# Kernel tuning notes

Measured on AMD Instinct MI355X. Metric: run time of the kernel, lower is better.

The kernel has to match this reference:

```python
import jax, jax.numpy as jnp
import numpy as np

B = 4          # per_gpu_batch_size
P = 16         # n_contexts
N = B * P      # fused passage dim = 64
L = 512        # seq_len
H = 768        # hidden_size
S = 16         # sentence spans per passage


def setup_inputs() -> dict:
    key = jax.random.key(0)
    k1, k2, k3 = jax.random.split(key, 3)
    hidden_states = jax.random.normal(k1, (N, L, H), jnp.float32)
    # nn.Linear weight [out, in]; original init std=1.0 saturates tanh, use 0.02 scale for sane numerics
    dense_w = jax.random.normal(k2, (H, H), jnp.float32) * 0.02
    dense_b = jnp.zeros((H,), jnp.float32)
    attention_mask = jnp.ones((N, L), jnp.int32)
    # strictly increasing boundaries -> S non-empty, ragged, contiguous spans per passage
    r = jnp.sort(jax.random.randint(k3, (N, S + 1), 0, L - S), axis=-1) + jnp.arange(S + 1, dtype=jnp.int32)
    spans = jnp.stack([r[:, :-1], r[:, 1:]], axis=-1).astype(jnp.int32)  # [N, S, 2]
    return dict(hidden_states=hidden_states, dense_w=dense_w, dense_b=dense_b,
                attention_mask=attention_mask, spans=spans)


def reference(hidden_states, dense_w, dense_b, attention_mask, spans):
    # sentence_spans branch: token_tensor = hidden_states (all tokens)
    # pooled_output = activation(dense(token_tensor)); cls_norm_type == 'none' -> no norm
    pooled = jnp.tanh(jnp.einsum('nlh,oh->nlo', hidden_states, dense_w) + dense_b)  # [N, L, H]
    pooled_output_passages = pooled[:, 0]  # [N, H]
    # ragged per-span mean pooling, vectorized as a masked segment reduce
    pos = jnp.arange(L, dtype=jnp.int32)                         # [L]
    start = spans[..., 0][..., None]                             # [N, S, 1]
    end = spans[..., 1][..., None]                               # [N, S, 1]
    m = ((pos >= start) & (pos < end)).astype(pooled.dtype)      # [N, S, L]
    sums = jnp.einsum('nsl,nlh->nsh', m, pooled)                 # [N, S, H]
    counts = (spans[..., 1] - spans[..., 0]).astype(pooled.dtype)[..., None]  # [N, S, 1]
    sentence_embeddings = (sums / counts).reshape(N * S, H)      # [N*S, H]
    # all S spans valid per passage -> mask of zeros (0 = valid in original code)
    sentence_mask = jnp.zeros((N, S), jnp.float32)
    return pooled_output_passages, sentence_embeddings, sentence_mask
```

## Files before the change

kernel.cpp:

```cpp
#include <hip/hip_runtime.h>
#include <hip/hip_bf16.h>

#define NPASS 64
#define LSEQ  512
#define HDIM  768
#define NSPAN 16
#define MTOT  (NPASS*LSEQ)
#define OFF_SENT (NPASS*HDIM)
#define OFF_MASK (OFF_SENT + NPASS*NSPAN*HDIM)
#define W_ELEMS (HDIM*HDIM)

#define BM   64
#define BK   32
#define NK   (HDIM/BK)
#define NBLK (MTOT/BM)
#define THREADS 512
#define NMT  2
#define NTN  12

typedef __bf16 bf16x8 __attribute__((ext_vector_type(8)));
typedef __bf16 bf16x4 __attribute__((ext_vector_type(4)));
typedef float  f32x4  __attribute__((ext_vector_type(4)));

__device__ inline unsigned short f2bf(float f) {
  __hip_bfloat16 h = __float2bfloat16(f);
  unsigned short u; __builtin_memcpy(&u, &h, 2); return u;
}

__device__ inline float fast_tanh(float x) {
  const float ax = fabsf(x);
  const float t  = __expf(-2.0f * ax);
  const float r  = (1.0f - t) * __builtin_amdgcn_rcpf(1.0f + t);
  return copysignf(r, x);
}

__device__ inline bf16x8 cvt8(f32x4 lo, f32x4 hi) {
  union { bf16x4 h[2]; bf16x8 v; } u;
  u.h[0] = __builtin_convertvector(lo, bf16x4);
  u.h[1] = __builtin_convertvector(hi, bf16x4);
  return u.v;
}

__global__ __launch_bounds__(256) void convert_w_kernel(
    const float* __restrict__ W, unsigned short* __restrict__ Wb)
{
  const int i = (blockIdx.x * 256 + threadIdx.x) * 8;
  const float4 a = *(const float4*)(W + i);
  const float4 b = *(const float4*)(W + i + 4);
  union { unsigned short us[8]; uint4 v; } o;
  o.us[0]=f2bf(a.x); o.us[1]=f2bf(a.y); o.us[2]=f2bf(a.z); o.us[3]=f2bf(a.w);
  o.us[4]=f2bf(b.x); o.us[5]=f2bf(b.y); o.us[6]=f2bf(b.z); o.us[7]=f2bf(b.w);
  *(uint4*)(Wb + i) = o.v;
}

__global__ __launch_bounds__(THREADS, 2) void gemm_fused_kernel(
    const float* __restrict__ A,
    const unsigned short* __restrict__ Wb,
    const float* __restrict__ bias,
    const int* __restrict__ spans,
    float* __restrict__ out)
{
  __shared__ __align__(16) float          As[2][BM*BK];
  __shared__ __align__(16) unsigned short Ws[2][HDIM*BK];
  __shared__ float inv_s[NSPAN];
  __shared__ float bias_s[HDIM];
  __shared__ short sid_l[BM];

  const int tid  = threadIdx.x;
  const int b    = blockIdx.x;
  const int p    = b >> 3;
  const int l0   = (b & 7) << 6;
  const int row0 = b * BM;

  const int wave = tid >> 6;
  const int lane = tid & 63;
  const int quad = lane >> 4;
  const int lr   = lane & 15;
  const int mr   = wave >> 2;
  const int nw   = wave & 3;

  auto stage = [&](int k, int buf) {
    const int k0 = k * BK;
    {
      const int row = wave * 8 + (lane >> 3);
      const int g   = (lane & 7) ^ ((lane >> 3) & 7);
      const float* src = A + (size_t)(row0 + row) * HDIM + (k0 + g * 4);
      __builtin_amdgcn_global_load_lds(
          (const __attribute__((address_space(1))) void*)src,
          (__attribute__((address_space(3))) void*)(As[buf] + wave * 256),
          16, 0, 0);
    }
    #pragma unroll
    for (int j = 0; j < 6; ++j) {
      const int s2  = wave * 6 + j;
      const int row = s2 * 16 + (lane >> 2);
      const int g   = (lane & 3) ^ ((lane >> 2) & 3);
      const unsigned short* src = Wb + (size_t)row * HDIM + (k0 + g * 8);
      __builtin_amdgcn_global_load_lds(
          (const __attribute__((address_space(1))) void*)src,
          (__attribute__((address_space(3))) void*)(Ws[buf] + s2 * 512),
          16, 0, 0);
    }
  };

  stage(0, 0);
  if (tid < NSPAN)
    inv_s[tid] = 1.0f / (float)(spans[(p * NSPAN + tid) * 2 + 1] -
                                spans[(p * NSPAN + tid) * 2 + 0]);
  if (tid < BM) {
    const int l = l0 + tid;
    short s = -1;
    #pragma unroll
    for (int i = 0; i < NSPAN; ++i) {
      const int st = spans[(p * NSPAN + i) * 2 + 0];
      const int en = spans[(p * NSPAN + i) * 2 + 1];
      if (l >= st && l < en) s = (short)i;
    }
    sid_l[tid] = s;
  }
  for (int i = tid; i < HDIM; i += THREADS) bias_s[i] = bias[i];
  __syncthreads();

  f32x4 acc[NMT][NTN];
  #pragma unroll
  for (int mt = 0; mt < NMT; ++mt)
    #pragma unroll
    for (int nt = 0; nt < NTN; ++nt)
      acc[mt][nt] = (f32x4){0.f, 0.f, 0.f, 0.f};

  for (int k = 0; k < NK; ++k) {
    const int cur = k & 1;
    if (k + 1 < NK) stage(k + 1, cur ^ 1);

    bf16x8 abf[NMT];
    #pragma unroll
    for (int mt = 0; mt < NMT; ++mt) {
      const int row = mr * 32 + mt * 16 + lr;
      const float* base = As[cur] + row * BK;
      const f32x4 lo = *(const f32x4*)(base + (((quad * 2    ) ^ (lr & 7)) * 4));
      const f32x4 hi = *(const f32x4*)(base + (((quad * 2 + 1) ^ (lr & 7)) * 4));
      abf[mt] = cvt8(lo, hi);
    }
    bf16x8 wf[NTN];
    #pragma unroll
    for (int nt = 0; nt < NTN; ++nt) {
      const int row = nw * 192 + nt * 16 + lr;
      wf[nt] = *(const bf16x8*)(Ws[cur] + row * BK + (quad ^ (lr & 3)) * 8);
    }

    __builtin_amdgcn_s_setprio(1);
    #pragma unroll
    for (int mt = 0; mt < NMT; ++mt)
      #pragma unroll
      for (int nt = 0; nt < NTN; ++nt)
        acc[mt][nt] = __builtin_amdgcn_mfma_f32_16x16x32_bf16(
            abf[mt], wf[nt], acc[mt][nt], 0, 0, 0);
    __builtin_amdgcn_s_setprio(0);

    __syncthreads();
  }

  #pragma unroll
  for (int nt = 0; nt < NTN; ++nt) {
    const int col = nw * 192 + nt * 16 + lr;
    const float bv = bias_s[col];
    float* sent_col = out + OFF_SENT + (size_t)(p * NSPAN) * HDIM + col;
    #pragma unroll
    for (int mt = 0; mt < NMT; ++mt) {
      const int rowbase = mr * 32 + mt * 16 + quad * 4;
      int prev = -1; float run = 0.f;
      #pragma unroll
      for (int r = 0; r < 4; ++r) {
        const int row = rowbase + r;
        const float v = fast_tanh(acc[mt][nt][r] + bv);
        if (l0 == 0 && row == 0) out[(size_t)p * HDIM + col] = v;
        const int s = sid_l[row];
        if (s != prev) {
          if (prev >= 0) unsafeAtomicAdd(sent_col + (size_t)prev * HDIM, run * inv_s[prev]);
          prev = s; run = 0.f;
        }
        run += v;
      }
      if (prev >= 0) unsafeAtomicAdd(sent_col + (size_t)prev * HDIM, run * inv_s[prev]);
    }
  }
}

extern "C" void kernel_launch(void* const* d_in, const int* in_sizes, int n_in,
                              void* d_out, int out_size, void* d_ws, size_t ws_size,
                              hipStream_t stream) {
  const float* hs  = (const float*)d_in[0];
  const float* w   = (const float*)d_in[1];
  const float* bsc = (const float*)d_in[2];
  const int* spans = (const int*)d_in[4];
  float* out = (float*)d_out;

  unsigned short* Wb = (unsigned short*)d_ws;

  hipMemsetAsync(d_out, 0, (size_t)out_size * sizeof(float), stream);

  convert_w_kernel<<<dim3(W_ELEMS / 8 / 256), dim3(256), 0, stream>>>(w, Wb);

  gemm_fused_kernel<<<dim3(NBLK), dim3(THREADS), 0, stream>>>(
      hs, Wb, bsc, spans, out);
}
```

Baseline: 281.1 us.

## Stage full A tile as bf16 in LDS and stream W directly from global into registers

The kernel now converts the block's whole 64x768 fp32 A tile to bf16 once into LDS, using an XOR swizzle, instead of double-buffering fp32 A and bf16 W slices per k-step. Each wave owns 96 output columns across all 64 rows and prefetches its W fragments from global/L2 straight into registers one k-step ahead. This removes the per-iteration __syncthreads and the LDS staging of W. In exchange, W is read redundantly from global by every block, the A load is no longer overlapped with compute, register pressure rises, and the fully unrolled k loop grows the code.

```diff
diff --git a/kernel.cpp b/kernel.cpp
--- a/kernel.cpp
+++ b/kernel.cpp
@@ -7,7 +7,6 @@
 #define NSPAN 16
 #define MTOT  (NPASS*LSEQ)
 #define OFF_SENT (NPASS*HDIM)
-#define OFF_MASK (OFF_SENT + NPASS*NSPAN*HDIM)
 #define W_ELEMS (HDIM*HDIM)
 
 #define BM   64
@@ -15,8 +14,9 @@
 #define NK   (HDIM/BK)
 #define NBLK (MTOT/BM)
 #define THREADS 512
-#define NMT  2
-#define NTN  12
+#define NMT  4
+#define NTN  6
+#define GPR  (HDIM/8)
 
 typedef __bf16 bf16x8 __attribute__((ext_vector_type(8)));
 typedef __bf16 bf16x4 __attribute__((ext_vector_type(4)));
@@ -53,15 +53,14 @@
   *(uint4*)(Wb + i) = o.v;
 }
 
-__global__ __launch_bounds__(THREADS, 2) void gemm_fused_kernel(
+__global__ __launch_bounds__(THREADS, 2) void fused_kernel(
     const float* __restrict__ A,
     const unsigned short* __restrict__ Wb,
     const float* __restrict__ bias,
-    const int* __restrict__ spans,
+    const int*   __restrict__ spans,
     float* __restrict__ out)
 {
-  __shared__ __align__(16) float          As[2][BM*BK];
-  __shared__ __align__(16) unsigned short Ws[2][HDIM*BK];
+  __shared__ __align__(16) unsigned short Al[BM * HDIM];
   __shared__ float inv_s[NSPAN];
   __shared__ float bias_s[HDIM];
   __shared__ short sid_l[BM];
@@ -76,37 +75,20 @@
   const int lane = tid & 63;
   const int quad = lane >> 4;
   const int lr   = lane & 15;
-  const int mr   = wave >> 2;
-  const int nw   = wave & 3;
 
-  auto stage = [&](int k, int buf) {
-    const int k0 = k * BK;
-    {
-      const int row = wave * 8 + (lane >> 3);
-      const int g   = (lane & 7) ^ ((lane >> 3) & 7);
-      const float* src = A + (size_t)(row0 + row) * HDIM + (k0 + g * 4);
-      __builtin_amdgcn_global_load_lds(
-          (const __attribute__((address_space(1))) void*)src,
-          (__attribute__((address_space(3))) void*)(As[buf] + wave * 256),
-          16, 0, 0);
+  {
+    #pragma unroll
+    for (int j = 0; j < (BM * GPR) / THREADS; ++j) {
+      const int g  = j * THREADS + tid;
+      const int r  = g / GPR;
+      const int kg = g % GPR;
+      const float* src = A + (size_t)(row0 + r) * HDIM + kg * 8;
+      const f32x4 lo = *(const f32x4*)src;
+      const f32x4 hi = *(const f32x4*)(src + 4);
+      *(bf16x8*)(Al + (size_t)r * HDIM + ((kg ^ (r & 7)) * 8)) = cvt8(lo, hi);
     }
-    #pragma unroll
-    for (int j = 0; j < 6; ++j) {
-      const int s2  = wave * 6 + j;
-      const int row = s2 * 16 + (lane >> 2);
-      const int g   = (lane & 3) ^ ((lane >> 2) & 3);
-      const unsigned short* src = Wb + (size_t)row * HDIM + (k0 + g * 8);
-      __builtin_amdgcn_global_load_lds(
-          (const __attribute__((address_space(1))) void*)src,
-          (__attribute__((address_space(3))) void*)(Ws[buf] + s2 * 512),
-          16, 0, 0);
-    }
-  };
+  }
 
-  stage(0, 0);
-  if (tid < NSPAN)
-    inv_s[tid] = 1.0f / (float)(spans[(p * NSPAN + tid) * 2 + 1] -
-                                spans[(p * NSPAN + tid) * 2 + 0]);
   if (tid < BM) {
     const int l = l0 + tid;
     short s = -1;
@@ -118,8 +100,15 @@
     }
     sid_l[tid] = s;
   }
+  if (tid < NSPAN)
+    inv_s[tid] = 1.0f / (float)(spans[(p * NSPAN + tid) * 2 + 1] -
+                                spans[(p * NSPAN + tid) * 2 + 0]);
   for (int i = tid; i < HDIM; i += THREADS) bias_s[i] = bias[i];
+
   __syncthreads();
+
+  const unsigned short* Wp =
+      Wb + (size_t)(wave * 96 + lr) * HDIM + quad * 8;
 
   f32x4 acc[NMT][NTN];
   #pragma unroll
@@ -128,46 +117,45 @@
     for (int nt = 0; nt < NTN; ++nt)
       acc[mt][nt] = (f32x4){0.f, 0.f, 0.f, 0.f};
 
+  bf16x8 w_cur[NTN], w_nxt[NTN];
+  #pragma unroll
+  for (int nt = 0; nt < NTN; ++nt)
+    w_cur[nt] = *(const bf16x8*)(Wp + (size_t)nt * 16 * HDIM);
+
+  #pragma unroll
   for (int k = 0; k < NK; ++k) {
-    const int cur = k & 1;
-    if (k + 1 < NK) stage(k + 1, cur ^ 1);
-
-    bf16x8 abf[NMT];
+    bf16x8 af[NMT];
     #pragma unroll
     for (int mt = 0; mt < NMT; ++mt) {
-      const int row = mr * 32 + mt * 16 + lr;
-      const float* base = As[cur] + row * BK;
-      const f32x4 lo = *(const f32x4*)(base + (((quad * 2    ) ^ (lr & 7)) * 4));
-      const f32x4 hi = *(const f32x4*)(base + (((quad * 2 + 1) ^ (lr & 7)) * 4));
-      abf[mt] = cvt8(lo, hi);
+      const int r  = mt * 16 + lr;
+      const int kg = (4 * k + quad) ^ (r & 7);
+      af[mt] = *(const bf16x8*)(Al + (size_t)r * HDIM + kg * 8);
     }
-    bf16x8 wf[NTN];
-    #pragma unroll
-    for (int nt = 0; nt < NTN; ++nt) {
-      const int row = nw * 192 + nt * 16 + lr;
-      wf[nt] = *(const bf16x8*)(Ws[cur] + row * BK + (quad ^ (lr & 3)) * 8);
+    if (k + 1 < NK) {
+      #pragma unroll
+      for (int nt = 0; nt < NTN; ++nt)
+        w_nxt[nt] = *(const bf16x8*)(Wp + (size_t)nt * 16 * HDIM + (k + 1) * BK);
     }
-
     __builtin_amdgcn_s_setprio(1);
     #pragma unroll
     for (int mt = 0; mt < NMT; ++mt)
       #pragma unroll
       for (int nt = 0; nt < NTN; ++nt)
         acc[mt][nt] = __builtin_amdgcn_mfma_f32_16x16x32_bf16(
-            abf[mt], wf[nt], acc[mt][nt], 0, 0, 0);
+            af[mt], w_cur[nt], acc[mt][nt], 0, 0, 0);
     __builtin_amdgcn_s_setprio(0);
-
-    __syncthreads();
+    #pragma unroll
+    for (int nt = 0; nt < NTN; ++nt) w_cur[nt] = w_nxt[nt];
   }
 
   #pragma unroll
   for (int nt = 0; nt < NTN; ++nt) {
-    const int col = nw * 192 + nt * 16 + lr;
+    const int col = wave * 96 + nt * 16 + lr;
     const float bv = bias_s[col];
     float* sent_col = out + OFF_SENT + (size_t)(p * NSPAN) * HDIM + col;
     #pragma unroll
     for (int mt = 0; mt < NMT; ++mt) {
-      const int rowbase = mr * 32 + mt * 16 + quad * 4;
+      const int rowbase = mt * 16 + quad * 4;
       int prev = -1; float run = 0.f;
       #pragma unroll
       for (int r = 0; r < 4; ++r) {
@@ -201,6 +189,6 @@
 
   convert_w_kernel<<<dim3(W_ELEMS / 8 / 256), dim3(256), 0, stream>>>(w, Wb);
 
-  gemm_fused_kernel<<<dim3(NBLK), dim3(THREADS), 0, stream>>>(
+  fused_kernel<<<dim3(NBLK), dim3(THREADS), 0, stream>>>(
       hs, Wb, bsc, spans, out);
 }
```

Measured after the change: 270.5 us. 1.04x faster.
